# Kernel tuning notes

Hardware: AMD Instinct MI355X
Metric: run time of the kernel (lower is better)

The kernel has to match this reference:

```python
import jax, jax.numpy as jnp
import numpy as np

B, S, H, V = 64, 512, 1024, 32000


def setup_inputs() -> dict:
    key = jax.random.key(0)
    ks = jax.random.split(key, 20)
    sd = 0.02
    inp = {
        'x': jax.random.randint(ks[0], (B, 1), 0, V),
        'h_prev': jax.random.normal(ks[1], (B, H), dtype=jnp.float32),
        'annotations': jax.random.normal(ks[2], (B, S, H), dtype=jnp.float32),
        # embedding table
        'emb': jax.random.normal(ks[3], (V, H), dtype=jnp.float32) * sd,
        # attention MLP: Linear(2H -> H), ReLU, Linear(H -> 1)
        'attn_W1': jax.random.normal(ks[4], (H, 2 * H), dtype=jnp.float32) * sd,
        'attn_b1': jnp.zeros((H,), jnp.float32),
        'attn_W2': jax.random.normal(ks[5], (1, H), dtype=jnp.float32) * sd,
        'attn_b2': jnp.zeros((1,), jnp.float32),
        # GRU cell linears (input_size = 2H). NOTE: original code has a bug where
        # weights_hr is never used (r uses weights_hz); we replicate that, so no Whr.
        'W_ir': jax.random.normal(ks[6], (H, 2 * H), dtype=jnp.float32) * sd,
        'b_ir': jnp.zeros((H,), jnp.float32),
        'W_iz': jax.random.normal(ks[7], (H, 2 * H), dtype=jnp.float32) * sd,
        'b_iz': jnp.zeros((H,), jnp.float32),
        'W_in': jax.random.normal(ks[8], (H, 2 * H), dtype=jnp.float32) * sd,
        'b_in': jnp.zeros((H,), jnp.float32),
        'W_hz': jax.random.normal(ks[9], (H, H), dtype=jnp.float32) * sd,
        'b_hz': jnp.zeros((H,), jnp.float32),
        'W_hn': jax.random.normal(ks[10], (H, H), dtype=jnp.float32) * sd,
        'b_hn': jnp.zeros((H,), jnp.float32),
        # output projection H -> V
        'W_out': jax.random.normal(ks[11], (V, H), dtype=jnp.float32) * sd,
        'b_out': jnp.zeros((V,), jnp.float32),
    }
    return inp


def _lin(x, W, b):
    # torch nn.Linear: y = x @ W.T + b, W has shape (out, in)
    return x @ W.T + b


def reference(x, h_prev, annotations, emb, attn_W1, attn_b1, attn_W2, attn_b2,
              W_ir, b_ir, W_iz, b_iz, W_in, b_in, W_hz, b_hz, W_hn, b_hn,
              W_out, b_out):
    # embedding lookup, squeeze time dim: (B, H)
    embed = emb[x[:, 0]]

    # additive attention: concat(annotations, expanded hidden) -> MLP -> softmax
    # split W1 over the concat axis to avoid materializing the [B,S,2H] concat:
    # concat @ W1.T == annotations @ W1[:, :H].T + hidden @ W1[:, H:].T
    hA = jnp.einsum('bsh,kh->bsk', annotations, attn_W1[:, :H])  # (B,S,H)
    hB = h_prev @ attn_W1[:, H:].T                               # (B,H)
    hidden_act = jax.nn.relu(hA + hB[:, None, :] + attn_b1)
    scores = jnp.einsum('bsk,k->bs', hidden_act, attn_W2[0]) + attn_b2[0]
    attention_weights = jax.nn.softmax(scores, axis=1)[:, :, None]  # (B,S,1)

    # context vector
    context = jnp.sum(attention_weights * annotations, axis=1)  # (B,H)
    xc = jnp.concatenate([context, embed], axis=1)              # (B,2H)

    # GRU cell (faithful to the original, including the weights_hz reuse in r)
    hz = _lin(h_prev, W_hz, b_hz)
    z = jax.nn.sigmoid(_lin(xc, W_iz, b_iz) + hz)
    r = jax.nn.sigmoid(_lin(xc, W_ir, b_ir) + hz)  # bug replicated: uses W_hz
    g = jnp.tanh(_lin(xc, W_in, b_in) + r * _lin(h_prev, W_hn, b_hn))
    h_new = (1.0 - z) * g + z * h_prev

    output = _lin(h_new, W_out, b_out)  # (B,V)
    return output, h_new, attention_weights
```

## Files before the change

kernel.cpp:

```cpp
#include <hip/hip_runtime.h>


typedef __bf16 bf16;
typedef __attribute__((ext_vector_type(4))) float  f32x4;
typedef __attribute__((ext_vector_type(4))) float  fx4;
typedef __attribute__((ext_vector_type(8))) bf16   bf16x8;
typedef __attribute__((ext_vector_type(4))) bf16   bf16x4;
typedef __attribute__((ext_vector_type(4))) unsigned int u32x4;
typedef __attribute__((ext_vector_type(2))) unsigned int u32x2;

#define MFMA16x16x32(a, b, c) __builtin_amdgcn_mfma_f32_16x16x32_bf16(a, b, c, 0, 0, 0)

#define Bb   64
#define Ss   512
#define Hh   1024
#define Vv   32000
#define Mtot (Bb * Ss)

#define WS_HPREV_B   0
#define WS_HNEW_B    131072
#define WS_XC_B      262144
#define WS_W1A_B     524288
#define WS_P_HB      2621440
#define WS_P_HZ      3670016
#define WS_P_HN      4718592
#define WS_P_IZ      5767168
#define WS_P_IR      6815744
#define WS_P_IN      7864320
#define WS_SCORES    8912896
#define WS_CTX       11010048
#define WS_ANNB      13107200

#define OUT_LOGITS   0
#define OUT_HNEW     2048000
#define OUT_AW       2113536

__device__ __forceinline__ float bf2f(unsigned short u) {
    unsigned int x = ((unsigned int)u) << 16;
    float f;
    __builtin_memcpy(&f, &x, 4);
    return f;
}

__device__ __forceinline__ void gload_lds16(const bf16* g, bf16* l)
{
    __builtin_amdgcn_global_load_lds(
        (const __attribute__((address_space(1))) unsigned int*)g,
        (__attribute__((address_space(3))) unsigned int*)l,
        16, 0, 0);
}

__global__ void k_prep(const int* __restrict__ x, const float* __restrict__ h_prev,
                       const float* __restrict__ emb, const float* __restrict__ attn_W1,
                       bf16* __restrict__ h_prev_b, bf16* __restrict__ xc_b,
                       bf16* __restrict__ W1a_b)
{
    int bid = blockIdx.x, t = threadIdx.x;
    if (bid < 64) {
        int b = bid;
        int row = x[b];
        for (int i = t; i < Hh; i += 256) {
            h_prev_b[b * Hh + i]          = (bf16)h_prev[b * Hh + i];
            xc_b[b * 2048 + Hh + i]       = (bf16)emb[(size_t)row * Hh + i];
        }
    } else {
        int row = bid - 64;
        int k4 = t * 4;
        fx4 v = *(const fx4*)(attn_W1 + (size_t)row * 2048 + k4);
        bf16x4 o;
#pragma unroll
        for (int q = 0; q < 4; q++) o[q] = (bf16)v[q];
        *(bf16x4*)(W1a_b + (size_t)row * Hh + k4) = o;
    }
}

__global__ void k_convann(const float* __restrict__ ann, bf16* __restrict__ annb)
{
    size_t i = ((size_t)blockIdx.x * 256 + threadIdx.x) * 8;
    size_t stride = (size_t)gridDim.x * 256 * 8;
    size_t n = (size_t)Mtot * Hh;
    for (; i < n; i += stride) {
        fx4 v0 = *(const fx4*)(ann + i);
        fx4 v1 = *(const fx4*)(ann + i + 4);
        bf16x8 o;
#pragma unroll
        for (int q = 0; q < 4; q++) { o[q] = (bf16)v0[q]; o[q + 4] = (bf16)v1[q]; }
        *(bf16x8*)(annb + i) = o;
    }
}

__global__ __launch_bounds__(256, 2) void k_sgemm(
    const bf16* __restrict__ A, int lda, int kchunk,
    const float* __restrict__ B0, const float* __restrict__ B1, const float* __restrict__ B2,
    int ldb0, int ldb1, int ldb2,
    float* __restrict__ o0, float* __restrict__ o1, float* __restrict__ o2,
    const float* __restrict__ bias, int N, int finalOut)
{
    __shared__ __align__(16) bf16 lA[2][64][72];
    __shared__ __align__(16) bf16 lB[2][64][72];

    int nb = blockIdx.x, sk = blockIdx.y, mat = blockIdx.z;
    const float* Bp = (mat == 0) ? B0 : (mat == 1 ? B1 : B2);
    int ldb         = (mat == 0) ? ldb0 : (mat == 1 ? ldb1 : ldb2);
    float* op       = (mat == 0) ? o0 : (mat == 1 ? o1 : o2);

    int n0 = nb * 64, k0 = sk * kchunk;
    int t = threadIdx.x, lane = t & 63, wid = t >> 6;
    int srow = t >> 2, schunk = t & 3;

    const bf16*  agp = A  + (size_t)srow * lda + k0 + schunk * 16;
    const float* bgp = Bp + (size_t)(n0 + srow) * ldb + k0 + schunk * 16;

    f32x4 acc[4];
#pragma unroll
    for (int i = 0; i < 4; i++) acc[i] = (f32x4)0.0f;

    u32x4 aR0, aR1; fx4 bRf[4];
    int nk = kchunk >> 6;

    aR0 = *(const u32x4*)(agp);
    aR1 = *(const u32x4*)(agp + 8);
#pragma unroll
    for (int q = 0; q < 4; q++) bRf[q] = *(const fx4*)(bgp + q * 4);
    {
        *(u32x4*)&lA[0][srow][schunk * 16]     = aR0;
        *(u32x4*)&lA[0][srow][schunk * 16 + 8] = aR1;
        bf16x8 p0, p1;
#pragma unroll
        for (int q = 0; q < 4; q++) {
            p0[q] = (bf16)bRf[0][q]; p0[q + 4] = (bf16)bRf[1][q];
            p1[q] = (bf16)bRf[2][q]; p1[q + 4] = (bf16)bRf[3][q];
        }
        *(bf16x8*)&lB[0][srow][schunk * 16]     = p0;
        *(bf16x8*)&lB[0][srow][schunk * 16 + 8] = p1;
    }
    __syncthreads();

    int cur = 0;
    for (int ks = 0; ks < nk; ks++) {
        if (ks + 1 < nk) {
            aR0 = *(const u32x4*)(agp + (ks + 1) * 64);
            aR1 = *(const u32x4*)(agp + (ks + 1) * 64 + 8);
#pragma unroll
            for (int q = 0; q < 4; q++) bRf[q] = *(const fx4*)(bgp + (ks + 1) * 64 + q * 4);
        }
        int rA = lane & 15;
        int kc = (lane >> 4) * 8;
#pragma unroll
        for (int kk = 0; kk < 2; kk++) {
            bf16x8 bfr = *(bf16x8*)&lB[cur][wid * 16 + rA][kk * 32 + kc];
#pragma unroll
            for (int i = 0; i < 4; i++) {
                bf16x8 af = *(bf16x8*)&lA[cur][i * 16 + rA][kk * 32 + kc];
                acc[i] = MFMA16x16x32(af, bfr, acc[i]);
            }
        }
        if (ks + 1 < nk) {
            int nxt = cur ^ 1;
            *(u32x4*)&lA[nxt][srow][schunk * 16]     = aR0;
            *(u32x4*)&lA[nxt][srow][schunk * 16 + 8] = aR1;
            bf16x8 p0, p1;
#pragma unroll
            for (int q = 0; q < 4; q++) {
                p0[q] = (bf16)bRf[0][q]; p0[q + 4] = (bf16)bRf[1][q];
                p1[q] = (bf16)bRf[2][q]; p1[q + 4] = (bf16)bRf[3][q];
            }
            *(bf16x8*)&lB[nxt][srow][schunk * 16]     = p0;
            *(bf16x8*)&lB[nxt][srow][schunk * 16 + 8] = p1;
        }
        __syncthreads();
        cur ^= 1;
    }

    int n = n0 + wid * 16 + (lane & 15);
#pragma unroll
    for (int i = 0; i < 4; i++) {
#pragma unroll
        for (int r = 0; r < 4; r++) {
            int m = i * 16 + (lane >> 4) * 4 + r;
            float v = acc[i][r];
            if (finalOut) op[(size_t)m * N + n] = v + bias[n];
            else          op[(size_t)(sk * 64 + m) * N + n] = v;
        }
    }
}

__global__ __launch_bounds__(512, 2) void k_attn(
    const bf16* __restrict__ annb, const bf16* __restrict__ Bw,
    const float* __restrict__ p_hB, const float* __restrict__ b1,
    const float* __restrict__ W2, float* __restrict__ scores_part)
{
    extern __shared__ char smem[];

    int bid = blockIdx.x;
    int wgid = (bid & 7) * 64 + (bid >> 3);
    int mb = wgid >> 2, nbp = wgid & 3;

    int t = threadIdx.x, lane = t & 63, wid = t >> 6;
    int wm = wid >> 2, wn = wid & 3;
    int r = lane & 15, q = lane >> 4;

    int srow = t >> 3;
    int gc   = (t & 7) ^ (srow & 7);
    size_t goff = (size_t)srow * 1024 + gc * 8;
    int doff = wid * 1024;

    const bf16* aSrc = annb + (size_t)mb * 262144;
    const bf16* bSrc = Bw   + (size_t)nbp * 262144;

    int rowAoff = (wm * 64 + r) * 128;
    int rowBoff = (wn * 32 + r) * 128;
    int e0 = (q ^ (r & 7)) * 16;
    int e1 = e0 ^ 64;

#define STAGEOP(src, half, buf, mat, kt) do {                                  \
        const bf16* s_ = (src) + (half) * 131072 + (size_t)(kt) * 64 + goff;   \
        char* d_ = smem + (buf) * 65536 + (mat) * 32768 + (half) * 16384 + doff; \
        gload_lds16(s_, (bf16*)d_);                                            \
        gload_lds16(s_ + 65536, (bf16*)(d_ + 8192));                           \
    } while (0)

#define VM4 asm volatile("s_waitcnt vmcnt(4)" ::: "memory")
#define VM0 asm volatile("s_waitcnt vmcnt(0)" ::: "memory")

    f32x4 acc[8][4];
#pragma unroll
    for (int i = 0; i < 8; i++)
#pragma unroll
        for (int j = 0; j < 4; j++) acc[i][j] = (f32x4)0.0f;

    bf16x8 bq[4];

#define PH(AH, KS, READB, STG, ENDW) do {                                      \
        const char* pa_ = smem + cur * 65536 + (AH) * 16384 + rowAoff;         \
        bf16x8 aq[4];                                                          \
        _Pragma("unroll")                                                      \
        for (int ip = 0; ip < 4; ip++)                                         \
            aq[ip] = *(const bf16x8*)(pa_ + ip * 2048 + ((KS) ? e1 : e0));     \
        if (READB) {                                                           \
            _Pragma("unroll")                                                  \
            for (int jp = 0; jp < 4; jp++) {                                   \
                const char* pb_ = smem + cur * 65536 + 32768                   \
                                + (jp >> 1) * 16384 + rowBoff;                 \
                bq[jp] = *(const bf16x8*)(pb_ + (jp & 1) * 2048 + ((KS) ? e1 : e0)); \
            }                                                                  \
        }                                                                      \
        STG;                                                                   \
        __builtin_amdgcn_s_barrier();                                          \
        __builtin_amdgcn_s_setprio(1);                                         \
        _Pragma("unroll")                                                      \
        for (int ip = 0; ip < 4; ip++)                                         \
            _Pragma("unroll")                                                  \
            for (int jp = 0; jp < 4; jp++)                                     \
                acc[(AH) * 4 + ip][jp] =                                       \
                    MFMA16x16x32(aq[ip], bq[jp], acc[(AH) * 4 + ip][jp]);      \
        __builtin_amdgcn_s_setprio(0);                                         \
        ENDW;                                                                  \
        __builtin_amdgcn_s_barrier();                                          \
    } while (0)

#define TILE(tt, S1, S2, VMW)                                                  \
        PH(0, 0, 1, if (S1) STAGEOP(aSrc, 1, nxt, 0, (tt) + 1), );             \
        PH(1, 0, 0, if (S1) STAGEOP(bSrc, 1, nxt, 1, (tt) + 1), );             \
        PH(0, 1, 1, , );                                                       \
        PH(1, 1, 0, if (S2) { STAGEOP(aSrc, 0, cur, 0, (tt) + 2);              \
                              STAGEOP(bSrc, 0, cur, 1, (tt) + 2); }, VMW);

    STAGEOP(aSrc, 0, 0, 0, 0);
    STAGEOP(bSrc, 0, 0, 1, 0);
    STAGEOP(aSrc, 1, 0, 0, 0);
    STAGEOP(bSrc, 1, 0, 1, 0);
    STAGEOP(aSrc, 0, 1, 0, 1);
    STAGEOP(bSrc, 0, 1, 1, 1);
    VM4;
    __builtin_amdgcn_s_barrier();

#pragma unroll 1
    for (int kt = 0; kt < 14; kt++) {
        int cur = kt & 1, nxt = cur ^ 1;
        TILE(kt, 1, 1, VM4);
    }
    {
        int cur = 0, nxt = 1;
        TILE(14, 1, 0, VM0);
    }
    {
        int cur = 1, nxt = 0;
        TILE(15, 0, 0, );
    }
#undef TILE
#undef PH
#undef STAGEOP

    int m0 = mb * 256, n0g = nbp * 256;
    int b = m0 >> 9;
    float hb[4], w2v[4];
#pragma unroll
    for (int j = 0; j < 4; j++) {
        int n = n0g + (j >> 1) * 128 + wn * 32 + (j & 1) * 16 + r;
        float h = p_hB[b * Hh + n] + p_hB[65536 + b * Hh + n]
                + p_hB[131072 + b * Hh + n] + p_hB[196608 + b * Hh + n];
        hb[j]  = h + b1[n];
        w2v[j] = W2[n];
    }
    float red[32];
#pragma unroll
    for (int i = 0; i < 8; i++)
#pragma unroll
        for (int rr = 0; rr < 4; rr++) {
            float s = 0.f;
#pragma unroll
            for (int j = 0; j < 4; j++) {
                float v = acc[i][j][rr] + hb[j];
                v = fmaxf(v, 0.f);
                s += v * w2v[j];
            }
            red[i * 4 + rr] = s;
        }
#pragma unroll
    for (int mask = 1; mask <= 8; mask <<= 1)
#pragma unroll
        for (int p = 0; p < 32; p++)
            red[p] += __shfl_xor(red[p], mask, 64);

    if (r == 0) {
        float* sp = scores_part + (size_t)(nbp * 4 + wn) * Mtot;
#pragma unroll
        for (int i = 0; i < 8; i++) {
            int m = m0 + wm * 64 + (i & 3) * 16 + (i >> 2) * 128 + q * 4;
#pragma unroll
            for (int rr = 0; rr < 4; rr++)
                sp[m + rr] = red[i * 4 + rr];
        }
    }
}

__global__ void k_softmax(const float* __restrict__ scores_part, float* __restrict__ aw)
{
    int b = blockIdx.x, s = threadIdx.x;
    int lane = s & 63, wid = s >> 6;
    float v = 0.f;
#pragma unroll
    for (int p = 0; p < 16; p++) v += scores_part[(size_t)p * Mtot + b * Ss + s];

    __shared__ float redm[8], redsum[8];
    float m = v;
#pragma unroll
    for (int mask = 32; mask; mask >>= 1) m = fmaxf(m, __shfl_xor(m, mask, 64));
    if (lane == 0) redm[wid] = m;
    __syncthreads();
    float bm = redm[0];
#pragma unroll
    for (int w = 1; w < 8; w++) bm = fmaxf(bm, redm[w]);

    float e = expf(v - bm);
    float ss = e;
#pragma unroll
    for (int mask = 32; mask; mask >>= 1) ss += __shfl_xor(ss, mask, 64);
    if (lane == 0) redsum[wid] = ss;
    __syncthreads();
    float tot = 0.f;
#pragma unroll
    for (int w = 0; w < 8; w++) tot += redsum[w];

    aw[b * Ss + s] = e / tot;
}

__global__ void k_context(const bf16* __restrict__ annb, const float* __restrict__ aw,
                          float* __restrict__ ctx_part)
{
    __shared__ float law[64];
    int bid = blockIdx.x;
    int b = bid >> 3, sc = bid & 7;
    int t = threadIdx.x;
    if (t < 64) law[t] = aw[b * Ss + sc * 64 + t];
    __syncthreads();
    int h0 = t * 4;
    const bf16* ap = annb + (size_t)(b * Ss + sc * 64) * Hh + h0;
    float a0 = 0, a1 = 0, a2 = 0, a3 = 0;
#pragma unroll 4
    for (int s2 = 0; s2 < 64; s2++) {
        float w = law[s2];
        u32x2 v = *(const u32x2*)(ap + (size_t)s2 * Hh);
        a0 += w * bf2f((unsigned short)(v[0] & 0xffff));
        a1 += w * bf2f((unsigned short)(v[0] >> 16));
        a2 += w * bf2f((unsigned short)(v[1] & 0xffff));
        a3 += w * bf2f((unsigned short)(v[1] >> 16));
    }
    fx4 o; o[0] = a0; o[1] = a1; o[2] = a2; o[3] = a3;
    *(fx4*)(ctx_part + sc * 65536 + b * Hh + h0) = o;
}

__global__ void k_xc(const float* __restrict__ ctx_part, bf16* __restrict__ xc_b)
{
    int idx = blockIdx.x * 256 + threadIdx.x;
    float c = 0.f;
#pragma unroll
    for (int p = 0; p < 8; p++) c += ctx_part[p * 65536 + idx];
    int b = idx >> 10, h = idx & 1023;
    xc_b[b * 2048 + h] = (bf16)c;
}

__global__ void k_gru(const float* __restrict__ p_iz, const float* __restrict__ p_ir,
                      const float* __restrict__ p_in, const float* __restrict__ p_hz,
                      const float* __restrict__ p_hn,
                      const float* __restrict__ b_iz, const float* __restrict__ b_ir,
                      const float* __restrict__ b_in, const float* __restrict__ b_hz,
                      const float* __restrict__ b_hn,
                      const float* __restrict__ h_prev,
                      float* __restrict__ out_h, bf16* __restrict__ h_new_b)
{
    int idx = blockIdx.x * 256 + threadIdx.x;
    int o = idx & 1023;
    float iz = p_iz[idx] + p_iz[65536 + idx] + p_iz[131072 + idx] + p_iz[196608 + idx];
    float ir = p_ir[idx] + p_ir[65536 + idx] + p_ir[131072 + idx] + p_ir[196608 + idx];
    float in_ = p_in[idx] + p_in[65536 + idx] + p_in[131072 + idx] + p_in[196608 + idx];
    float hz = p_hz[idx] + p_hz[65536 + idx] + p_hz[131072 + idx] + p_hz[196608 + idx];
    float hn = p_hn[idx] + p_hn[65536 + idx] + p_hn[131072 + idx] + p_hn[196608 + idx];
    hz += b_hz[o];
    hn += b_hn[o];
    float z = 1.f / (1.f + expf(-(iz + b_iz[o] + hz)));
    float r = 1.f / (1.f + expf(-(ir + b_ir[o] + hz)));
    float g = tanhf(in_ + b_in[o] + r * hn);
    float hp = h_prev[idx];
    float hnew = (1.f - z) * g + z * hp;
    out_h[idx] = hnew;
    h_new_b[idx] = (bf16)hnew;
}

extern "C" void kernel_launch(void* const* d_in, const int* in_sizes, int n_in,
                              void* d_out, int out_size, void* d_ws, size_t ws_size,
                              hipStream_t stream)
{
    const int*   x        = (const int*)d_in[0];
    const float* h_prev   = (const float*)d_in[1];
    const float* ann      = (const float*)d_in[2];
    const float* emb      = (const float*)d_in[3];
    const float* attn_W1  = (const float*)d_in[4];
    const float* attn_b1  = (const float*)d_in[5];
    const float* attn_W2  = (const float*)d_in[6];
    const float* W_ir     = (const float*)d_in[8];
    const float* b_ir     = (const float*)d_in[9];
    const float* W_iz     = (const float*)d_in[10];
    const float* b_iz     = (const float*)d_in[11];
    const float* W_in     = (const float*)d_in[12];
    const float* b_in     = (const float*)d_in[13];
    const float* W_hz     = (const float*)d_in[14];
    const float* b_hz     = (const float*)d_in[15];
    const float* W_hn     = (const float*)d_in[16];
    const float* b_hn     = (const float*)d_in[17];
    const float* W_out    = (const float*)d_in[18];
    const float* b_out    = (const float*)d_in[19];

    float* out = (float*)d_out;
    char*  ws  = (char*)d_ws;

    bf16*  h_prev_b = (bf16*)(ws + WS_HPREV_B);
    bf16*  h_new_b  = (bf16*)(ws + WS_HNEW_B);
    bf16*  xc_b     = (bf16*)(ws + WS_XC_B);
    bf16*  W1a_b    = (bf16*)(ws + WS_W1A_B);
    float* p_hB     = (float*)(ws + WS_P_HB);
    float* p_hz     = (float*)(ws + WS_P_HZ);
    float* p_hn     = (float*)(ws + WS_P_HN);
    float* p_iz     = (float*)(ws + WS_P_IZ);
    float* p_ir     = (float*)(ws + WS_P_IR);
    float* p_in     = (float*)(ws + WS_P_IN);
    float* scores_p = (float*)(ws + WS_SCORES);
    float* ctx_part = (float*)(ws + WS_CTX);
    bf16*  annb     = (bf16*)(ws + WS_ANNB);

    hipFuncSetAttribute(reinterpret_cast<const void*>(k_attn),
                        hipFuncAttributeMaxDynamicSharedMemorySize, 131072);

    k_prep<<<1088, 256, 0, stream>>>(x, h_prev, emb, attn_W1, h_prev_b, xc_b, W1a_b);
    k_convann<<<2048, 256, 0, stream>>>(ann, annb);

    {
        dim3 g(16, 4, 3);
        k_sgemm<<<g, 256, 0, stream>>>(h_prev_b, 1024, 256,
                                       attn_W1 + 1024, W_hz, W_hn, 2048, 1024, 1024,
                                       p_hB, p_hz, p_hn, nullptr, 1024, 0);
    }

    k_attn<<<512, 512, 131072, stream>>>(annb, W1a_b, p_hB, attn_b1, attn_W2, scores_p);

    k_softmax<<<64, 512, 0, stream>>>(scores_p, out + OUT_AW);

    k_context<<<512, 256, 0, stream>>>(annb, out + OUT_AW, ctx_part);

    k_xc<<<256, 256, 0, stream>>>(ctx_part, xc_b);

    {
        dim3 g(16, 4, 3);
        k_sgemm<<<g, 256, 0, stream>>>(xc_b, 2048, 512,
                                       W_iz, W_ir, W_in, 2048, 2048, 2048,
                                       p_iz, p_ir, p_in, nullptr, 1024, 0);
    }

    k_gru<<<256, 256, 0, stream>>>(p_iz, p_ir, p_in, p_hz, p_hn,
                                   b_iz, b_ir, b_in, b_hz, b_hn,
                                   h_prev, out + OUT_HNEW, h_new_b);

    {
        dim3 g(500, 1, 1);
        k_sgemm<<<g, 256, 0, stream>>>(h_new_b, 1024, 1024,
                                       W_out, W_out, W_out, 1024, 1024, 1024,
                                       out + OUT_LOGITS, nullptr, nullptr,
                                       b_out, 32000, 1);
    }
}
```

Baseline: 173.6 us.

## Fuse fp32-to-bf16 annotation conversion into attention GEMM A-tile staging

Removes the separate k_convann kernel. The attention GEMM now loads fp32 annotations into registers, converts them to bf16, and writes them into swizzled LDS, with the next tile's global loads overlapping the current compute. The nbp==0 blocks also write the bf16 copy out for the later context kernel. This drops one full fp32 read and bf16 write pass plus a launch. In exchange, each attention block reads fp32 A (twice the bytes, repeated across the 4 N-blocks), holds more registers, and replaces async global-to-LDS copies with register staging, which may weaken the pipeline.

```diff
diff --git a/kernel.cpp b/kernel.cpp
--- a/kernel.cpp
+++ b/kernel.cpp
@@ -74,21 +74,6 @@
     }
 }
 
-__global__ void k_convann(const float* __restrict__ ann, bf16* __restrict__ annb)
-{
-    size_t i = ((size_t)blockIdx.x * 256 + threadIdx.x) * 8;
-    size_t stride = (size_t)gridDim.x * 256 * 8;
-    size_t n = (size_t)Mtot * Hh;
-    for (; i < n; i += stride) {
-        fx4 v0 = *(const fx4*)(ann + i);
-        fx4 v1 = *(const fx4*)(ann + i + 4);
-        bf16x8 o;
-#pragma unroll
-        for (int q = 0; q < 4; q++) { o[q] = (bf16)v0[q]; o[q + 4] = (bf16)v1[q]; }
-        *(bf16x8*)(annb + i) = o;
-    }
-}
-
 __global__ __launch_bounds__(256, 2) void k_sgemm(
     const bf16* __restrict__ A, int lda, int kchunk,
     const float* __restrict__ B0, const float* __restrict__ B1, const float* __restrict__ B2,
@@ -186,9 +171,10 @@
 }
 
 __global__ __launch_bounds__(512, 2) void k_attn(
-    const bf16* __restrict__ annb, const bf16* __restrict__ Bw,
+    const float* __restrict__ ann, const bf16* __restrict__ Bw,
     const float* __restrict__ p_hB, const float* __restrict__ b1,
-    const float* __restrict__ W2, float* __restrict__ scores_part)
+    const float* __restrict__ W2, float* __restrict__ scores_part,
+    bf16* __restrict__ annb)
 {
     extern __shared__ char smem[];
 
@@ -201,27 +187,52 @@
     int r = lane & 15, q = lane >> 4;
 
     int srow = t >> 3;
-    int gc   = (t & 7) ^ (srow & 7);
+    int gc = (t & 7) ^ (srow & 7);
     size_t goff = (size_t)srow * 1024 + gc * 8;
     int doff = wid * 1024;
-
-    const bf16* aSrc = annb + (size_t)mb * 262144;
-    const bf16* bSrc = Bw   + (size_t)nbp * 262144;
+    const bf16* bSrc = Bw + (size_t)nbp * 262144;
+
+    int rs = t >> 2, cs = t & 3;
+    int rx = rs & 7;
+    int cpos0 = ((cs * 2) ^ rx) * 16;
+    int cpos1 = ((cs * 2 + 1) ^ rx) * 16;
+    const float* aG = ann  + (size_t)(mb * 256 + rs) * 1024 + cs * 16;
+    bf16*        wbG = annb + (size_t)(mb * 256 + rs) * 1024 + cs * 16;
+    int awoff = rs * 128;
 
     int rowAoff = (wm * 64 + r) * 128;
     int rowBoff = (wn * 32 + r) * 128;
     int e0 = (q ^ (r & 7)) * 16;
     int e1 = e0 ^ 64;
 
-#define STAGEOP(src, half, buf, mat, kt) do {                                  \
-        const bf16* s_ = (src) + (half) * 131072 + (size_t)(kt) * 64 + goff;   \
-        char* d_ = smem + (buf) * 65536 + (mat) * 32768 + (half) * 16384 + doff; \
+#define VMW(n) asm volatile("s_waitcnt vmcnt(" #n ")" ::: "memory")
+#define LGKM0  asm volatile("s_waitcnt lgkmcnt(0)" ::: "memory")
+
+#define BSTAGE(half, buf, kt) do {                                             \
+        const bf16* s_ = bSrc + (half) * 131072 + (size_t)(kt) * 64 + goff;    \
+        char* d_ = smem + (buf) * 65536 + 32768 + (half) * 16384 + doff;       \
         gload_lds16(s_, (bf16*)d_);                                            \
-        gload_lds16(s_ + 65536, (bf16*)(d_ + 8192));                           \
-    } while (0)
-
-#define VM4 asm volatile("s_waitcnt vmcnt(4)" ::: "memory")
-#define VM0 asm volatile("s_waitcnt vmcnt(0)" ::: "memory")
+        gload_lds16(s_ + 65536, (bf16*)(d_ + 8192)); } while (0)
+
+#define ALOAD(half, kt) do {                                                   \
+        const fx4* s_ = (const fx4*)(aG + (half) * 131072 + (size_t)(kt) * 64);\
+        aF[(half)*4+0] = s_[0]; aF[(half)*4+1] = s_[1];                        \
+        aF[(half)*4+2] = s_[2]; aF[(half)*4+3] = s_[3]; } while (0)
+
+#define ASTORE(half, buf, kt) do {                                             \
+        bf16x8 w0, w1;                                                         \
+        _Pragma("unroll")                                                      \
+        for (int z = 0; z < 4; z++) {                                          \
+            w0[z] = (bf16)aF[(half)*4+0][z]; w0[z+4] = (bf16)aF[(half)*4+1][z];\
+            w1[z] = (bf16)aF[(half)*4+2][z]; w1[z+4] = (bf16)aF[(half)*4+3][z];\
+        }                                                                      \
+        char* d_ = smem + (buf) * 65536 + (half) * 16384 + awoff;              \
+        *(bf16x8*)(d_ + cpos0) = w0;                                           \
+        *(bf16x8*)(d_ + cpos1) = w1;                                           \
+        if (nbp == 0) {                                                        \
+            bf16* g_ = wbG + (half) * 131072 + (size_t)(kt) * 64;              \
+            *(bf16x8*)g_ = w0; *(bf16x8*)(g_ + 8) = w1;                        \
+        } } while (0)
 
     f32x4 acc[8][4];
 #pragma unroll
@@ -229,9 +240,10 @@
 #pragma unroll
         for (int j = 0; j < 4; j++) acc[i][j] = (f32x4)0.0f;
 
+    fx4 aF[8];
     bf16x8 bq[4];
 
-#define PH(AH, KS, READB, STG, ENDW) do {                                      \
+#define PH(AH, KS, READB, STG) do {                                            \
         const char* pa_ = smem + cur * 65536 + (AH) * 16384 + rowAoff;         \
         bf16x8 aq[4];                                                          \
         _Pragma("unroll")                                                      \
@@ -255,42 +267,51 @@
                 acc[(AH) * 4 + ip][jp] =                                       \
                     MFMA16x16x32(aq[ip], bq[jp], acc[(AH) * 4 + ip][jp]);      \
         __builtin_amdgcn_s_setprio(0);                                         \
-        ENDW;                                                                  \
         __builtin_amdgcn_s_barrier();                                          \
     } while (0)
 
-#define TILE(tt, S1, S2, VMW)                                                  \
-        PH(0, 0, 1, if (S1) STAGEOP(aSrc, 1, nxt, 0, (tt) + 1), );             \
-        PH(1, 0, 0, if (S1) STAGEOP(bSrc, 1, nxt, 1, (tt) + 1), );             \
-        PH(0, 1, 1, , );                                                       \
-        PH(1, 1, 0, if (S2) { STAGEOP(aSrc, 0, cur, 0, (tt) + 2);              \
-                              STAGEOP(bSrc, 0, cur, 1, (tt) + 2); }, VMW);
-
-    STAGEOP(aSrc, 0, 0, 0, 0);
-    STAGEOP(bSrc, 0, 0, 1, 0);
-    STAGEOP(aSrc, 1, 0, 0, 0);
-    STAGEOP(bSrc, 1, 0, 1, 0);
-    STAGEOP(aSrc, 0, 1, 0, 1);
-    STAGEOP(bSrc, 0, 1, 1, 1);
-    VM4;
+    ALOAD(0, 0); ALOAD(1, 0);
+    BSTAGE(0, 0, 0); BSTAGE(1, 0, 0);
+    BSTAGE(0, 1, 1); BSTAGE(1, 1, 1);
+    VMW(8);
+    ASTORE(0, 0, 0); ASTORE(1, 0, 0);
+    ALOAD(0, 1); ALOAD(1, 1);
+    VMW(8);
+    LGKM0;
     __builtin_amdgcn_s_barrier();
 
 #pragma unroll 1
-    for (int kt = 0; kt < 14; kt++) {
+    for (int kt = 0; kt < 16; kt++) {
         int cur = kt & 1, nxt = cur ^ 1;
-        TILE(kt, 1, 1, VM4);
-    }
-    {
-        int cur = 0, nxt = 1;
-        TILE(14, 1, 0, VM0);
-    }
-    {
-        int cur = 1, nxt = 0;
-        TILE(15, 0, 0, );
-    }
-#undef TILE
+        PH(0, 0, 1, );
+        PH(1, 0, 0, );
+        PH(0, 1, 1, );
+        if (kt < 14) {
+            PH(1, 1, 0, {
+                VMW(0);
+                ASTORE(0, nxt, kt + 1);
+                ASTORE(1, nxt, kt + 1);
+                BSTAGE(0, cur, kt + 2);
+                BSTAGE(1, cur, kt + 2);
+                ALOAD(0, kt + 2);
+                ALOAD(1, kt + 2);
+                LGKM0;
+            });
+        } else if (kt == 14) {
+            PH(1, 1, 0, {
+                VMW(0);
+                ASTORE(0, nxt, 15);
+                ASTORE(1, nxt, 15);
+                LGKM0;
+            });
+        } else {
+            PH(1, 1, 0, );
+        }
+    }
 #undef PH
-#undef STAGEOP
+#undef ASTORE
+#undef ALOAD
+#undef BSTAGE
 
     int m0 = mb * 256, n0g = nbp * 256;
     int b = m0 >> 9;
@@ -473,7 +494,6 @@
                         hipFuncAttributeMaxDynamicSharedMemorySize, 131072);
 
     k_prep<<<1088, 256, 0, stream>>>(x, h_prev, emb, attn_W1, h_prev_b, xc_b, W1a_b);
-    k_convann<<<2048, 256, 0, stream>>>(ann, annb);
 
     {
         dim3 g(16, 4, 3);
@@ -482,7 +502,8 @@
                                        p_hB, p_hz, p_hn, nullptr, 1024, 0);
     }
 
-    k_attn<<<512, 512, 131072, stream>>>(annb, W1a_b, p_hB, attn_b1, attn_W2, scores_p);
+    k_attn<<<512, 512, 131072, stream>>>(ann, W1a_b, p_hB, attn_b1, attn_W2,
+                                         scores_p, annb);
 
     k_softmax<<<64, 512, 0, stream>>>(scores_p, out + OUT_AW);
 
```

Result: slower. 269.1 us (+55.0%).
